# Performance work log

Hardware: AMD Instinct MI355X
Metric: run time of the kernel (lower is better)

## Reference

```python
import jax, jax.numpy as jnp
import numpy as np

IN_DIM = 512
OUT_DIM = 512


def setup_inputs() -> dict:
    key = jax.random.key(0)
    ks = jax.random.split(key, 7)
    B, S = 4, 2048
    scale = 1.0 / np.sqrt(IN_DIM)
    X = jax.random.normal(ks[0], (B, S, IN_DIM), dtype=jnp.float32)
    Wq = jax.random.normal(ks[1], (IN_DIM, OUT_DIM), dtype=jnp.float32) * scale
    Wk = jax.random.normal(ks[2], (IN_DIM, OUT_DIM), dtype=jnp.float32) * scale
    Wv = jax.random.normal(ks[3], (IN_DIM, OUT_DIM), dtype=jnp.float32) * scale
    bq = jnp.zeros((OUT_DIM,), dtype=jnp.float32)
    bk = jnp.zeros((OUT_DIM,), dtype=jnp.float32)
    bv = jnp.zeros((OUT_DIM,), dtype=jnp.float32)
    return {"X": X, "Wq": Wq, "bq": bq, "Wk": Wk, "bk": bk, "Wv": Wv, "bv": bv}


def reference(X, Wq, bq, Wk, bk, Wv, bv):
    # Q/K/V projections: [B,S,in] @ [in,out] -> [B,S,out]
    Q = X @ Wq + bq
    K = X @ Wk + bk
    V = X @ Wv + bv
    d_k = jnp.asarray(Q.shape[-1], Q.dtype)
    # scores: [B,S,S] = QK^T / sqrt(d_k)
    scores = jnp.einsum('bsd,btd->bst', Q, K) / jnp.sqrt(d_k)
    attn = jax.nn.softmax(scores, axis=-1)
    # out: [B,S,out]
    return jnp.einsum('bst,btd->bsd', attn, V)
```

## Files before the change

kernel.cpp:

```cpp
#include <hip/hip_runtime.h>
#include <hip/hip_bf16.h>
#include <stdint.h>

#define SEQ   2048
#define DIM   512
#define BATCH 4

typedef __attribute__((ext_vector_type(8))) short  short8;
typedef __attribute__((ext_vector_type(4))) float  floatx4;

static __device__ __forceinline__ unsigned short f2b(float f) {
  return __builtin_bit_cast(unsigned short, __float2bfloat16(f));
}

static __device__ __forceinline__ void gll16(const void* g, void* l) {
  __builtin_amdgcn_global_load_lds(
      (__attribute__((address_space(1))) void*)(uintptr_t)g,
      (__attribute__((address_space(3))) void*)l, 16, 0, 0);
}


template <int AF, int BF, int WM, int WN, int KC, int PH, int KIT>
__device__ __forceinline__ void fgemm_8p(
    const char* __restrict__ A, int rtA0, int TKA,
    const char* __restrict__ B, int rtB0, int TKB,
    char* lds, floatx4 (&acc)[AF / WM][BF / WN])
{
  constexpr int AWF  = AF / WM, BWF = BF / WN;
  constexpr int SLOT = (AF + BF) * KC * 1024;
  constexpr int L    = KC * (AF / 8 + BF / 8);
  constexpr int AC   = AWF / PH;
  static_assert(KIT >= 3, "pipeline needs >=3 K-slots");
  static_assert(AWF % PH == 0 && L % PH == 0, "phase split must divide");
  const int tid = threadIdx.x;
  const int w = tid >> 6, l = tid & 63;
  const int wm = w % WM, wn = w / WM;

  auto stage_part = [&](int slot, int kt, int p) {
    char* dst = lds + slot * SLOT;
#pragma unroll
    for (int g = p * (L / PH); g < (p + 1) * (L / PH); ++g) {
      if (g < KC * (AF / 8)) {
        const int c = g / (AF / 8), q = g % (AF / 8);
        const int f = q * 8 + w;
        gll16(A + (((size_t)(rtA0 + f) * TKA + kt * KC + c) << 10) + l * 16,
              dst + (c * AF + f) * 1024 + l * 16);
      } else {
        const int h = g - KC * (AF / 8);
        const int c = h / (BF / 8), q = h % (BF / 8);
        const int f = q * 8 + w;
        gll16(B + (((size_t)(rtB0 + f) * TKB + kt * KC + c) << 10) + l * 16,
              dst + (KC * AF + c * BF + f) * 1024 + l * 16);
      }
    }
  };
  auto stage_all = [&](int slot, int kt) {
#pragma unroll
    for (int p = 0; p < PH; ++p) stage_part(slot, kt, p);
  };

  stage_all(0, 0); stage_all(1, 1); stage_all(2, 2);
  asm volatile("s_waitcnt vmcnt(%0) lgkmcnt(0)\ns_barrier" :: "n"(2 * L) : "memory");

  short8 bf[KC][BWF];
#pragma unroll 4
  for (int kt = 0; kt < KIT; ++kt) {
    const char* bA = lds + (kt & 3) * SLOT;
    const char* bB = bA + KC * AF * 1024;
#pragma unroll
    for (int p = 0; p < PH; ++p) {
      short8 af[KC][AC];
#pragma unroll
      for (int c = 0; c < KC; ++c)
#pragma unroll
        for (int i = 0; i < AC; ++i)
          af[c][i] = *(const short8*)(bA + (c * AF + wm * AWF + p * AC + i) * 1024 + l * 16);
      if (p == 0) {
#pragma unroll
        for (int c = 0; c < KC; ++c)
#pragma unroll
          for (int j = 0; j < BWF; ++j)
            bf[c][j] = *(const short8*)(bB + (c * BF + wn * BWF + j) * 1024 + l * 16);
      }
      if (kt + 3 < KIT) stage_part((kt + 3) & 3, kt + 3, p);

      asm volatile("s_barrier" ::: "memory");
      asm volatile("s_waitcnt lgkmcnt(0)" ::: "memory");
      __builtin_amdgcn_s_setprio(1);
#pragma unroll
      for (int c = 0; c < KC; ++c)
#pragma unroll
        for (int i = 0; i < AC; ++i)
#pragma unroll
          for (int j = 0; j < BWF; ++j)
            acc[p * AC + i][j] = __builtin_amdgcn_mfma_f32_16x16x32_bf16(
                af[c][i], bf[c][j], acc[p * AC + i][j], 0, 0, 0);
      __builtin_amdgcn_s_setprio(0);

      if (p == PH - 1) {
        if (kt + 3 < KIT)
          asm volatile("s_waitcnt vmcnt(%0)\ns_barrier" :: "n"(2 * L) : "memory");
        else if (kt + 2 < KIT)
          asm volatile("s_waitcnt vmcnt(%0)\ns_barrier" :: "n"(L) : "memory");
        else if (kt + 1 < KIT)
          asm volatile("s_waitcnt vmcnt(0)\ns_barrier" ::: "memory");
      } else {
        asm volatile("s_barrier" ::: "memory");
      }
    }
  }
}

__global__ __launch_bounds__(256) void setup_kernel(
    const float* __restrict__ X, const float* __restrict__ Wq,
    const float* __restrict__ Wk, const float* __restrict__ Wv,
    short8* __restrict__ XbF, short8* __restrict__ WF,
    float* __restrict__ rowsum)
{
  const int flat = blockIdx.x * 256 + threadIdx.x;
  {
    const int tile = flat >> 6, l = flat & 63;
    const int row = (tile >> 4) * 16 + (l & 15);
    const int k0  = (tile & 15) * 32 + (l >> 4) * 8;
    const float4 v0 = *(const float4*)(X + (size_t)row * DIM + k0);
    const float4 v1 = *(const float4*)(X + (size_t)row * DIM + k0 + 4);
    short8 o;
    o[0] = (short)f2b(v0.x); o[1] = (short)f2b(v0.y);
    o[2] = (short)f2b(v0.z); o[3] = (short)f2b(v0.w);
    o[4] = (short)f2b(v1.x); o[5] = (short)f2b(v1.y);
    o[6] = (short)f2b(v1.z); o[7] = (short)f2b(v1.w);
    XbF[flat] = o;
  }
  if (flat < 3 * 32768) {
    const int z = flat >> 15, within = flat & 32767;
    const float* W = (z == 0) ? Wq : (z == 1) ? Wk : Wv;
    const int tile = within >> 6, l = within & 63;
    const int n  = (tile >> 4) * 16 + (l & 15);
    const int k0 = (tile & 15) * 32 + (l >> 4) * 8;
    short8 o;
#pragma unroll
    for (int e = 0; e < 8; ++e)
      o[e] = (short)f2b(W[(size_t)(k0 + e) * DIM + n]);
    WF[flat] = o;
  }
  if (flat < 2048) ((float4*)rowsum)[flat] = float4{0.f, 0.f, 0.f, 0.f};
}

__global__ __launch_bounds__(512, 2) void qkv_kernel(
    const short8* __restrict__ XbF, const short8* __restrict__ WF,
    const float* __restrict__ bq, const float* __restrict__ bk,
    const float* __restrict__ bv,
    unsigned short* __restrict__ QF, unsigned short* __restrict__ KF,
    unsigned short* __restrict__ VF)
{
  __shared__ char lds[131072];
  const int z = blockIdx.z, job = blockIdx.x;
  const int lane = threadIdx.x & 63, w = threadIdx.x >> 6;
  const int wm = w & 1, wn = w >> 1;
  const int x = job & 31, y = job >> 5;
  const char* Xc = (const char*)XbF;
  const char* Wc = (const char*)WF;
  floatx4 acc[8][4] = {};

  if (z < 2) {
    fgemm_8p<16, 16, 2, 4, 1, 2, 16>(Wc + (size_t)z * 524288, y * 16, 16,
                                     Xc, x * 16, 16, lds, acc);
    const float* bias = z ? bk : bq;
    unsigned short* OF = z ? KF : QF;
    const int dbase = y * 256 + wm * 128;
    const int sbase = x * 256 + wn * 64;
#pragma unroll
    for (int i = 0; i < 8; ++i) {
      const int d0 = dbase + i * 16 + (lane >> 4) * 4;
      const float4 b4 = *(const float4*)(bias + d0);
#pragma unroll
      for (int j = 0; j < 4; ++j) {
        const int s = sbase + j * 16 + (lane & 15);
        ushort4 pk;
        pk.x = f2b(acc[i][j][0] + b4.x);
        pk.y = f2b(acc[i][j][1] + b4.y);
        pk.z = f2b(acc[i][j][2] + b4.z);
        pk.w = f2b(acc[i][j][3] + b4.w);
        *(ushort4*)(OF + (size_t)((s >> 4) * 16 + (d0 >> 5)) * 512 +
                    ((((d0 & 31) >> 3) << 4) | (s & 15)) * 8 + (d0 & 7)) = pk;
      }
    }
  } else {
    fgemm_8p<16, 16, 2, 4, 1, 2, 16>(Xc, x * 16, 16,
                                     Wc + 2 * 524288, y * 16, 16, lds, acc);
    const int sbase = x * 256 + wm * 128;
    const int dbase = y * 256 + wn * 64;
#pragma unroll
    for (int i = 0; i < 8; ++i) {
      const int s0 = sbase + i * 16 + (lane >> 4) * 4;
      const int bt = s0 >> 11, t0 = s0 & 2047;
#pragma unroll
      for (int j = 0; j < 4; ++j) {
        const int d = dbase + j * 16 + (lane & 15);
        const float bn = bv[d];
        ushort4 pk;
        pk.x = f2b(acc[i][j][0] + bn);
        pk.y = f2b(acc[i][j][1] + bn);
        pk.z = f2b(acc[i][j][2] + bn);
        pk.w = f2b(acc[i][j][3] + bn);
        *(ushort4*)(VF + (size_t)bt * DIM * SEQ +
                    (size_t)((d >> 4) * 64 + (t0 >> 5)) * 512 +
                    ((((t0 & 31) >> 3) << 4) | (d & 15)) * 8 + (t0 & 7)) = pk;
      }
    }
  }
}

__global__ __launch_bounds__(512, 2) void scores_kernel(
    const unsigned short* __restrict__ QF, const unsigned short* __restrict__ KF,
    unsigned short* __restrict__ ScF, float* __restrict__ rowsum)
{
  __shared__ char lds[131072];
  const int b = blockIdx.z, x = blockIdx.x, y = blockIdx.y;
  const int lane = threadIdx.x & 63, w = threadIdx.x >> 6;
  const int wm = w & 1, wn = w >> 1;
  floatx4 acc[8][4] = {};
  fgemm_8p<16, 16, 2, 4, 1, 2, 16>((const char*)KF + (size_t)b * 2097152, y * 16, 16,
                                   (const char*)QF + (size_t)b * 2097152, x * 16, 16,
                                   lds, acc);

  unsigned short* S = ScF + (size_t)b * SEQ * SEQ;
  const float scale = 0.044194173824159216f;
  const int tbase = y * 256 + wm * 128;
  const int sbase = x * 256 + wn * 64;
  float colsum[4] = {0.f, 0.f, 0.f, 0.f};
#pragma unroll
  for (int i = 0; i < 8; ++i) {
    const int t0 = tbase + i * 16 + (lane >> 4) * 4;
#pragma unroll
    for (int j = 0; j < 4; ++j) {
      const int s = sbase + j * 16 + (lane & 15);
      float e0 = __expf(acc[i][j][0] * scale);
      float e1 = __expf(acc[i][j][1] * scale);
      float e2 = __expf(acc[i][j][2] * scale);
      float e3 = __expf(acc[i][j][3] * scale);
      colsum[j] += (e0 + e1) + (e2 + e3);
      ushort4 pk;
      pk.x = f2b(e0); pk.y = f2b(e1); pk.z = f2b(e2); pk.w = f2b(e3);
      *(ushort4*)(S + (size_t)((s >> 4) * 64 + (t0 >> 5)) * 512 +
                  ((((t0 & 31) >> 3) << 4) | (s & 15)) * 8 + (t0 & 7)) = pk;
    }
  }
#pragma unroll
  for (int j = 0; j < 4; ++j) {
    colsum[j] += __shfl_xor(colsum[j], 16, 64);
    colsum[j] += __shfl_xor(colsum[j], 32, 64);
  }
  if (lane < 16) {
#pragma unroll
    for (int j = 0; j < 4; ++j)
      atomicAdd(rowsum + b * SEQ + sbase + j * 16 + lane, colsum[j]);
  }
}

__global__ __launch_bounds__(512, 2) void pv_kernel(
    const unsigned short* __restrict__ ScF, const unsigned short* __restrict__ VF,
    const float* __restrict__ rowsum, float* __restrict__ out)
{
  __shared__ char lds[131072];
  const int b = blockIdx.z, x = blockIdx.x, y = blockIdx.y;
  const int lane = threadIdx.x & 63, w = threadIdx.x >> 6;
  const int wm = w & 1, wn = w >> 1;
  floatx4 acc[4][2] = {};
  fgemm_8p<8, 8, 2, 4, 2, 1, 32>((const char*)ScF + (size_t)b * 8388608, x * 8, 64,
                                 (const char*)VF + (size_t)b * 2097152, y * 8, 64,
                                 lds, acc);

  const int mbase = x * 128 + wm * 64;
  const int dbase = y * 128 + wn * 32;
#pragma unroll
  for (int i = 0; i < 4; ++i) {
    const int m0 = mbase + i * 16 + (lane >> 4) * 4;
    const float4 rs = *(const float4*)(rowsum + b * SEQ + m0);
    const float inv0 = 1.f / rs.x, inv1 = 1.f / rs.y, inv2 = 1.f / rs.z, inv3 = 1.f / rs.w;
#pragma unroll
    for (int j = 0; j < 2; ++j) {
      const int d = dbase + j * 16 + (lane & 15);
      float* o = out + ((size_t)b * SEQ + m0) * DIM + d;
      o[0 * DIM] = acc[i][j][0] * inv0;
      o[1 * DIM] = acc[i][j][1] * inv1;
      o[2 * DIM] = acc[i][j][2] * inv2;
      o[3 * DIM] = acc[i][j][3] * inv3;
    }
  }
}

extern "C" void kernel_launch(void* const* d_in, const int* in_sizes, int n_in,
                              void* d_out, int out_size, void* d_ws, size_t ws_size,
                              hipStream_t stream) {
  const float* X  = (const float*)d_in[0];
  const float* Wq = (const float*)d_in[1];
  const float* bq = (const float*)d_in[2];
  const float* Wk = (const float*)d_in[3];
  const float* bk = (const float*)d_in[4];
  const float* Wv = (const float*)d_in[5];
  const float* bv = (const float*)d_in[6];
  float* out = (float*)d_out;
  char* ws = (char*)d_ws;

  short8* XbF = (short8*)(ws + 0);
  short8* WF  = (short8*)(ws + 8388608);
  char*   QF  = ws + 9961472;
  char*   KF  = ws + 18350080;
  char*   VF  = ws + 26738688;
  char*   ScF = ws + 35127296;
  float*  rowsum = (float*)(ws + 68681728);

  setup_kernel<<<dim3(2048), 256, 0, stream>>>(X, Wq, Wk, Wv, XbF, WF, rowsum);
  qkv_kernel<<<dim3(64, 1, 3), 512, 0, stream>>>(
      XbF, WF, bq, bk, bv,
      (unsigned short*)QF, (unsigned short*)KF, (unsigned short*)VF);
  scores_kernel<<<dim3(8, 8, 4), 512, 0, stream>>>(
      (const unsigned short*)QF, (const unsigned short*)KF,
      (unsigned short*)ScF, rowsum);
  pv_kernel<<<dim3(16, 4, 4), 512, 0, stream>>>(
      (const unsigned short*)ScF, (const unsigned short*)VF, rowsum, out);
}
```

Baseline: 140.7 us.

## Fuse attention stages into one cooperative persistent kernel with grid syncs

The four kernels (conversion, QKV projection, scores plus exp, PV) become a single cooperative kernel of 256 blocks that separates the stages with grid-wide syncs, removing launch gaps between kernels. Row sums no longer use atomicAdd into a zeroed buffer: each block writes partial sums into a buffer that reuses the space of the bf16 X copy, and the PV stage reduces the 16 partials into reciprocals in LDS. The old multi-kernel path is kept as a fallback if the cooperative launch fails. In exchange, idle blocks during the QKV stage and the cost of grid syncs must be absorbed, and every block must fit co-resident.

```diff
diff --git a/kernel.cpp b/kernel.cpp
--- a/kernel.cpp
+++ b/kernel.cpp
@@ -1,6 +1,9 @@
 #include <hip/hip_runtime.h>
 #include <hip/hip_bf16.h>
+#include <hip/hip_cooperative_groups.h>
 #include <stdint.h>
+
+namespace cg = cooperative_groups;
 
 #define SEQ   2048
 #define DIM   512
@@ -111,11 +114,216 @@
   }
 }
 
+
+static __device__ __forceinline__ void do_setup(
+    int blk, const float* __restrict__ X, const float* __restrict__ Wq,
+    const float* __restrict__ Wk, const float* __restrict__ Wv,
+    short8* __restrict__ XbF, short8* __restrict__ WF)
+{
+#pragma unroll
+  for (int u = 0; u < 4; ++u) {
+    const int flat = blk * 2048 + u * 512 + (int)threadIdx.x;
+    const int tile = flat >> 6, l = flat & 63;
+    const int row = (tile >> 4) * 16 + (l & 15);
+    const int k0  = (tile & 15) * 32 + (l >> 4) * 8;
+    const float4 v0 = *(const float4*)(X + (size_t)row * DIM + k0);
+    const float4 v1 = *(const float4*)(X + (size_t)row * DIM + k0 + 4);
+    short8 o;
+    o[0] = (short)f2b(v0.x); o[1] = (short)f2b(v0.y);
+    o[2] = (short)f2b(v0.z); o[3] = (short)f2b(v0.w);
+    o[4] = (short)f2b(v1.x); o[5] = (short)f2b(v1.y);
+    o[6] = (short)f2b(v1.z); o[7] = (short)f2b(v1.w);
+    XbF[flat] = o;
+  }
+  const int fl = blk * 512 + (int)threadIdx.x;
+  if (fl < 3 * 32768) {
+    const int z = fl >> 15, within = fl & 32767;
+    const float* W = (z == 0) ? Wq : (z == 1) ? Wk : Wv;
+    const int tile = within >> 6, l = within & 63;
+    const int n  = (tile >> 4) * 16 + (l & 15);
+    const int k0 = (tile & 15) * 32 + (l >> 4) * 8;
+    short8 o;
+#pragma unroll
+    for (int e = 0; e < 8; ++e)
+      o[e] = (short)f2b(W[(size_t)(k0 + e) * DIM + n]);
+    WF[fl] = o;
+  }
+}
+
+static __device__ __forceinline__ void do_qkv(
+    int z, int job, char* lds, const short8* __restrict__ XbF,
+    const short8* __restrict__ WF, const float* __restrict__ bq,
+    const float* __restrict__ bk, const float* __restrict__ bv,
+    unsigned short* __restrict__ QF, unsigned short* __restrict__ KF,
+    unsigned short* __restrict__ VF)
+{
+  const int lane = threadIdx.x & 63, w = threadIdx.x >> 6;
+  const int wm = w & 1, wn = w >> 1;
+  const int x = job & 31, y = job >> 5;
+  const char* Xc = (const char*)XbF;
+  const char* Wc = (const char*)WF;
+  floatx4 acc[8][4] = {};
+
+  if (z < 2) {
+    fgemm_8p<16, 16, 2, 4, 1, 2, 16>(Wc + (size_t)z * 524288, y * 16, 16,
+                                     Xc, x * 16, 16, lds, acc);
+    const float* bias = z ? bk : bq;
+    unsigned short* OF = z ? KF : QF;
+    const int dbase = y * 256 + wm * 128;
+    const int sbase = x * 256 + wn * 64;
+#pragma unroll
+    for (int i = 0; i < 8; ++i) {
+      const int d0 = dbase + i * 16 + (lane >> 4) * 4;
+      const float4 b4 = *(const float4*)(bias + d0);
+#pragma unroll
+      for (int j = 0; j < 4; ++j) {
+        const int s = sbase + j * 16 + (lane & 15);
+        ushort4 pk;
+        pk.x = f2b(acc[i][j][0] + b4.x);
+        pk.y = f2b(acc[i][j][1] + b4.y);
+        pk.z = f2b(acc[i][j][2] + b4.z);
+        pk.w = f2b(acc[i][j][3] + b4.w);
+        *(ushort4*)(OF + (size_t)((s >> 4) * 16 + (d0 >> 5)) * 512 +
+                    ((((d0 & 31) >> 3) << 4) | (s & 15)) * 8 + (d0 & 7)) = pk;
+      }
+    }
+  } else {
+    fgemm_8p<16, 16, 2, 4, 1, 2, 16>(Xc, x * 16, 16,
+                                     Wc + 2 * 524288, y * 16, 16, lds, acc);
+    const int sbase = x * 256 + wm * 128;
+    const int dbase = y * 256 + wn * 64;
+#pragma unroll
+    for (int i = 0; i < 8; ++i) {
+      const int s0 = sbase + i * 16 + (lane >> 4) * 4;
+      const int bt = s0 >> 11, t0 = s0 & 2047;
+#pragma unroll
+      for (int j = 0; j < 4; ++j) {
+        const int d = dbase + j * 16 + (lane & 15);
+        const float bn = bv[d];
+        ushort4 pk;
+        pk.x = f2b(acc[i][j][0] + bn);
+        pk.y = f2b(acc[i][j][1] + bn);
+        pk.z = f2b(acc[i][j][2] + bn);
+        pk.w = f2b(acc[i][j][3] + bn);
+        *(ushort4*)(VF + (size_t)bt * DIM * SEQ +
+                    (size_t)((d >> 4) * 64 + (t0 >> 5)) * 512 +
+                    ((((t0 & 31) >> 3) << 4) | (d & 15)) * 8 + (t0 & 7)) = pk;
+      }
+    }
+  }
+}
+
+static __device__ __forceinline__ void do_scores(
+    int b, int x, int y, char* lds, const unsigned short* __restrict__ QF,
+    const unsigned short* __restrict__ KF, unsigned short* __restrict__ ScF,
+    float* __restrict__ prow)
+{
+  const int lane = threadIdx.x & 63, w = threadIdx.x >> 6;
+  const int wm = w & 1, wn = w >> 1;
+  floatx4 acc[8][4] = {};
+  fgemm_8p<16, 16, 2, 4, 1, 2, 16>((const char*)KF + (size_t)b * 2097152, y * 16, 16,
+                                   (const char*)QF + (size_t)b * 2097152, x * 16, 16,
+                                   lds, acc);
+
+  unsigned short* S = ScF + (size_t)b * SEQ * SEQ;
+  const float scale = 0.044194173824159216f;
+  const int tbase = y * 256 + wm * 128;
+  const int sbase = x * 256 + wn * 64;
+  float colsum[4] = {0.f, 0.f, 0.f, 0.f};
+#pragma unroll
+  for (int i = 0; i < 8; ++i) {
+    const int t0 = tbase + i * 16 + (lane >> 4) * 4;
+#pragma unroll
+    for (int j = 0; j < 4; ++j) {
+      const int s = sbase + j * 16 + (lane & 15);
+      float e0 = __expf(acc[i][j][0] * scale);
+      float e1 = __expf(acc[i][j][1] * scale);
+      float e2 = __expf(acc[i][j][2] * scale);
+      float e3 = __expf(acc[i][j][3] * scale);
+      colsum[j] += (e0 + e1) + (e2 + e3);
+      ushort4 pk;
+      pk.x = f2b(e0); pk.y = f2b(e1); pk.z = f2b(e2); pk.w = f2b(e3);
+      *(ushort4*)(S + (size_t)((s >> 4) * 64 + (t0 >> 5)) * 512 +
+                  ((((t0 & 31) >> 3) << 4) | (s & 15)) * 8 + (t0 & 7)) = pk;
+    }
+  }
+#pragma unroll
+  for (int j = 0; j < 4; ++j) {
+    colsum[j] += __shfl_xor(colsum[j], 16, 64);
+    colsum[j] += __shfl_xor(colsum[j], 32, 64);
+  }
+  if (lane < 16) {
+    float* dst = prow + ((size_t)(y * 2 + wm) * BATCH + b) * SEQ + sbase + lane;
+#pragma unroll
+    for (int j = 0; j < 4; ++j) dst[j * 16] = colsum[j];
+  }
+}
+
+static __device__ __forceinline__ void do_pv(
+    int b, int x, int y, char* lds, float* rinv,
+    const unsigned short* __restrict__ ScF, const unsigned short* __restrict__ VF,
+    const float* __restrict__ prow, float* __restrict__ out)
+{
+  const int t = threadIdx.x;
+  if (t < 128) {
+    const int s = x * 128 + t;
+    float r = 0.f;
+#pragma unroll
+    for (int q = 0; q < 16; ++q) r += prow[((size_t)q * BATCH + b) * SEQ + s];
+    rinv[t] = 1.f / r;
+  }
+  const int lane = threadIdx.x & 63, w = threadIdx.x >> 6;
+  const int wm = w & 1, wn = w >> 1;
+  floatx4 acc[4][2] = {};
+  fgemm_8p<8, 8, 2, 4, 2, 1, 32>((const char*)ScF + (size_t)b * 8388608, x * 8, 64,
+                                 (const char*)VF + (size_t)b * 2097152, y * 8, 64,
+                                 lds, acc);
+
+  const int mbase = x * 128 + wm * 64;
+  const int dbase = y * 128 + wn * 32;
+#pragma unroll
+  for (int i = 0; i < 4; ++i) {
+    const int r0 = wm * 64 + i * 16 + (lane >> 4) * 4;
+    const int m0 = mbase + i * 16 + (lane >> 4) * 4;
+    const float inv0 = rinv[r0], inv1 = rinv[r0 + 1], inv2 = rinv[r0 + 2], inv3 = rinv[r0 + 3];
+#pragma unroll
+    for (int j = 0; j < 2; ++j) {
+      const int d = dbase + j * 16 + (lane & 15);
+      float* o = out + ((size_t)b * SEQ + m0) * DIM + d;
+      o[0 * DIM] = acc[i][j][0] * inv0;
+      o[1 * DIM] = acc[i][j][1] * inv1;
+      o[2 * DIM] = acc[i][j][2] * inv2;
+      o[3 * DIM] = acc[i][j][3] * inv3;
+    }
+  }
+}
+
+__global__ __launch_bounds__(512, 2) void mega_kernel(
+    const float* X, const float* Wq, const float* Wk, const float* Wv,
+    const float* bq, const float* bk, const float* bv,
+    short8* XbF, short8* WF, unsigned short* QF, unsigned short* KF,
+    unsigned short* VF, unsigned short* ScF, float* prow, float* out)
+{
+  __shared__ char lds[131072];
+  __shared__ float rinv[128];
+  cg::grid_group grid = cg::this_grid();
+  const int blk = blockIdx.x;
+
+  do_setup(blk, X, Wq, Wk, Wv, XbF, WF);
+  grid.sync();
+  if (blk < 192) do_qkv(blk >> 6, blk & 63, lds, XbF, WF, bq, bk, bv, QF, KF, VF);
+  grid.sync();
+  { const int b = blk >> 6, r = blk & 63;
+    do_scores(b, r & 7, r >> 3, lds, QF, KF, ScF, prow); }
+  grid.sync();
+  { const int b = blk >> 6, r = blk & 63;
+    do_pv(b, r >> 2, r & 3, lds, rinv, ScF, VF, prow, out); }
+}
+
 __global__ __launch_bounds__(256) void setup_kernel(
     const float* __restrict__ X, const float* __restrict__ Wq,
     const float* __restrict__ Wk, const float* __restrict__ Wv,
-    short8* __restrict__ XbF, short8* __restrict__ WF,
-    float* __restrict__ rowsum)
+    short8* __restrict__ XbF, short8* __restrict__ WF)
 {
   const int flat = blockIdx.x * 256 + threadIdx.x;
   {
@@ -143,7 +351,6 @@
       o[e] = (short)f2b(W[(size_t)(k0 + e) * DIM + n]);
     WF[flat] = o;
   }
-  if (flat < 2048) ((float4*)rowsum)[flat] = float4{0.f, 0.f, 0.f, 0.f};
 }
 
 __global__ __launch_bounds__(512, 2) void qkv_kernel(
@@ -154,140 +361,24 @@
     unsigned short* __restrict__ VF)
 {
   __shared__ char lds[131072];
-  const int z = blockIdx.z, job = blockIdx.x;
-  const int lane = threadIdx.x & 63, w = threadIdx.x >> 6;
-  const int wm = w & 1, wn = w >> 1;
-  const int x = job & 31, y = job >> 5;
-  const char* Xc = (const char*)XbF;
-  const char* Wc = (const char*)WF;
-  floatx4 acc[8][4] = {};
-
-  if (z < 2) {
-    fgemm_8p<16, 16, 2, 4, 1, 2, 16>(Wc + (size_t)z * 524288, y * 16, 16,
-                                     Xc, x * 16, 16, lds, acc);
-    const float* bias = z ? bk : bq;
-    unsigned short* OF = z ? KF : QF;
-    const int dbase = y * 256 + wm * 128;
-    const int sbase = x * 256 + wn * 64;
-#pragma unroll
-    for (int i = 0; i < 8; ++i) {
-      const int d0 = dbase + i * 16 + (lane >> 4) * 4;
-      const float4 b4 = *(const float4*)(bias + d0);
-#pragma unroll
-      for (int j = 0; j < 4; ++j) {
-        const int s = sbase + j * 16 + (lane & 15);
-        ushort4 pk;
-        pk.x = f2b(acc[i][j][0] + b4.x);
-        pk.y = f2b(acc[i][j][1] + b4.y);
-        pk.z = f2b(acc[i][j][2] + b4.z);
-        pk.w = f2b(acc[i][j][3] + b4.w);
-        *(ushort4*)(OF + (size_t)((s >> 4) * 16 + (d0 >> 5)) * 512 +
-                    ((((d0 & 31) >> 3) << 4) | (s & 15)) * 8 + (d0 & 7)) = pk;
-      }
-    }
-  } else {
-    fgemm_8p<16, 16, 2, 4, 1, 2, 16>(Xc, x * 16, 16,
-                                     Wc + 2 * 524288, y * 16, 16, lds, acc);
-    const int sbase = x * 256 + wm * 128;
-    const int dbase = y * 256 + wn * 64;
-#pragma unroll
-    for (int i = 0; i < 8; ++i) {
-      const int s0 = sbase + i * 16 + (lane >> 4) * 4;
-      const int bt = s0 >> 11, t0 = s0 & 2047;
-#pragma unroll
-      for (int j = 0; j < 4; ++j) {
-        const int d = dbase + j * 16 + (lane & 15);
-        const float bn = bv[d];
-        ushort4 pk;
-        pk.x = f2b(acc[i][j][0] + bn);
-        pk.y = f2b(acc[i][j][1] + bn);
-        pk.z = f2b(acc[i][j][2] + bn);
-        pk.w = f2b(acc[i][j][3] + bn);
-        *(ushort4*)(VF + (size_t)bt * DIM * SEQ +
-                    (size_t)((d >> 4) * 64 + (t0 >> 5)) * 512 +
-                    ((((t0 & 31) >> 3) << 4) | (d & 15)) * 8 + (t0 & 7)) = pk;
-      }
-    }
-  }
+  do_qkv(blockIdx.z, blockIdx.x, lds, XbF, WF, bq, bk, bv, QF, KF, VF);
 }
 
 __global__ __launch_bounds__(512, 2) void scores_kernel(
     const unsigned short* __restrict__ QF, const unsigned short* __restrict__ KF,
-    unsigned short* __restrict__ ScF, float* __restrict__ rowsum)
+    unsigned short* __restrict__ ScF, float* __restrict__ prow)
 {
   __shared__ char lds[131072];
-  const int b = blockIdx.z, x = blockIdx.x, y = blockIdx.y;
-  const int lane = threadIdx.x & 63, w = threadIdx.x >> 6;
-  const int wm = w & 1, wn = w >> 1;
-  floatx4 acc[8][4] = {};
-  fgemm_8p<16, 16, 2, 4, 1, 2, 16>((const char*)KF + (size_t)b * 2097152, y * 16, 16,
-                                   (const char*)QF + (size_t)b * 2097152, x * 16, 16,
-                                   lds, acc);
-
-  unsigned short* S = ScF + (size_t)b * SEQ * SEQ;
-  const float scale = 0.044194173824159216f;
-  const int tbase = y * 256 + wm * 128;
-  const int sbase = x * 256 + wn * 64;
-  float colsum[4] = {0.f, 0.f, 0.f, 0.f};
-#pragma unroll
-  for (int i = 0; i < 8; ++i) {
-    const int t0 = tbase + i * 16 + (lane >> 4) * 4;
-#pragma unroll
-    for (int j = 0; j < 4; ++j) {
-      const int s = sbase + j * 16 + (lane & 15);
-      float e0 = __expf(acc[i][j][0] * scale);
-      float e1 = __expf(acc[i][j][1] * scale);
-      float e2 = __expf(acc[i][j][2] * scale);
-      float e3 = __expf(acc[i][j][3] * scale);
-      colsum[j] += (e0 + e1) + (e2 + e3);
-      ushort4 pk;
-      pk.x = f2b(e0); pk.y = f2b(e1); pk.z = f2b(e2); pk.w = f2b(e3);
-      *(ushort4*)(S + (size_t)((s >> 4) * 64 + (t0 >> 5)) * 512 +
-                  ((((t0 & 31) >> 3) << 4) | (s & 15)) * 8 + (t0 & 7)) = pk;
-    }
-  }
-#pragma unroll
-  for (int j = 0; j < 4; ++j) {
-    colsum[j] += __shfl_xor(colsum[j], 16, 64);
-    colsum[j] += __shfl_xor(colsum[j], 32, 64);
-  }
-  if (lane < 16) {
-#pragma unroll
-    for (int j = 0; j < 4; ++j)
-      atomicAdd(rowsum + b * SEQ + sbase + j * 16 + lane, colsum[j]);
-  }
+  do_scores(blockIdx.z, blockIdx.x, blockIdx.y, lds, QF, KF, ScF, prow);
 }
 
 __global__ __launch_bounds__(512, 2) void pv_kernel(
     const unsigned short* __restrict__ ScF, const unsigned short* __restrict__ VF,
-    const float* __restrict__ rowsum, float* __restrict__ out)
+    const float* __restrict__ prow, float* __restrict__ out)
 {
   __shared__ char lds[131072];
-  const int b = blockIdx.z, x = blockIdx.x, y = blockIdx.y;
-  const int lane = threadIdx.x & 63, w = threadIdx.x >> 6;
-  const int wm = w & 1, wn = w >> 1;
-  floatx4 acc[4][2] = {};
-  fgemm_8p<8, 8, 2, 4, 2, 1, 32>((const char*)ScF + (size_t)b * 8388608, x * 8, 64,
-                                 (const char*)VF + (size_t)b * 2097152, y * 8, 64,
-                                 lds, acc);
-
-  const int mbase = x * 128 + wm * 64;
-  const int dbase = y * 128 + wn * 32;
-#pragma unroll
-  for (int i = 0; i < 4; ++i) {
-    const int m0 = mbase + i * 16 + (lane >> 4) * 4;
-    const float4 rs = *(const float4*)(rowsum + b * SEQ + m0);
-    const float inv0 = 1.f / rs.x, inv1 = 1.f / rs.y, inv2 = 1.f / rs.z, inv3 = 1.f / rs.w;
-#pragma unroll
-    for (int j = 0; j < 2; ++j) {
-      const int d = dbase + j * 16 + (lane & 15);
-      float* o = out + ((size_t)b * SEQ + m0) * DIM + d;
-      o[0 * DIM] = acc[i][j][0] * inv0;
-      o[1 * DIM] = acc[i][j][1] * inv1;
-      o[2 * DIM] = acc[i][j][2] * inv2;
-      o[3 * DIM] = acc[i][j][3] * inv3;
-    }
-  }
+  __shared__ float rinv[128];
+  do_pv(blockIdx.z, blockIdx.x, blockIdx.y, lds, rinv, ScF, VF, prow, out);
 }
 
 extern "C" void kernel_launch(void* const* d_in, const int* in_sizes, int n_in,
@@ -304,20 +395,26 @@
   char* ws = (char*)d_ws;
 
   short8* XbF = (short8*)(ws + 0);
+  float*  prow = (float*)(ws + 0);
   short8* WF  = (short8*)(ws + 8388608);
-  char*   QF  = ws + 9961472;
-  char*   KF  = ws + 18350080;
-  char*   VF  = ws + 26738688;
-  char*   ScF = ws + 35127296;
-  float*  rowsum = (float*)(ws + 68681728);
-
-  setup_kernel<<<dim3(2048), 256, 0, stream>>>(X, Wq, Wk, Wv, XbF, WF, rowsum);
-  qkv_kernel<<<dim3(64, 1, 3), 512, 0, stream>>>(
-      XbF, WF, bq, bk, bv,
-      (unsigned short*)QF, (unsigned short*)KF, (unsigned short*)VF);
-  scores_kernel<<<dim3(8, 8, 4), 512, 0, stream>>>(
-      (const unsigned short*)QF, (const unsigned short*)KF,
-      (unsigned short*)ScF, rowsum);
-  pv_kernel<<<dim3(16, 4, 4), 512, 0, stream>>>(
-      (const unsigned short*)ScF, (const unsigned short*)VF, rowsum, out);
-}
+  unsigned short* QF  = (unsigned short*)(ws + 9961472);
+  unsigned short* KF  = (unsigned short*)(ws + 18350080);
+  unsigned short* VF  = (unsigned short*)(ws + 26738688);
+  unsigned short* ScF = (unsigned short*)(ws + 35127296);
+
+  void* args[] = {
+    (void*)&X, (void*)&Wq, (void*)&Wk, (void*)&Wv,
+    (void*)&bq, (void*)&bk, (void*)&bv,
+    (void*)&XbF, (void*)&WF, (void*)&QF, (void*)&KF,
+    (void*)&VF, (void*)&ScF, (void*)&prow, (void*)&out
+  };
+  hipError_t e = hipLaunchCooperativeKernel(
+      (const void*)mega_kernel, dim3(256), dim3(512), args, 0, stream);
+  if (e != hipSuccess) {
+    (void)hipGetLastError();
+    setup_kernel<<<dim3(2048), 256, 0, stream>>>(X, Wq, Wk, Wv, XbF, WF);
+    qkv_kernel<<<dim3(64, 1, 3), 512, 0, stream>>>(XbF, WF, bq, bk, bv, QF, KF, VF);
+    scores_kernel<<<dim3(8, 8, 4), 512, 0, stream>>>(QF, KF, ScF, prow);
+    pv_kernel<<<dim3(16, 4, 4), 512, 0, stream>>>(ScF, VF, prow, out);
+  }
+}
```

Measured after the change: 260.8 us. 1.85x slower.

## Remap grids for XCD-local L2 reuse and replace rowsum atomics with partial sums

Applied to the files above, without the earlier changes.

Flattens the grids of the qkv, scores and pv kernels into 1D and remaps block indices so that blocks sharing operands (same batch, same rows) land on the same XCD, which is meant to improve L2 reuse. The scores kernel now writes per-tile partial row sums into a buffer instead of using atomicAdd, and pv reduces those 16 partials per row into LDS before the GEMM. This drops the zeroing step in setup and the atomic traffic. In exchange, the partial-sum buffer reuses the XbF workspace region, which is safe only because XbF is dead after qkv, and pv does some extra global reads.

```diff
diff --git a/kernel.cpp b/kernel.cpp
--- a/kernel.cpp
+++ b/kernel.cpp
@@ -114,8 +114,7 @@
 __global__ __launch_bounds__(256) void setup_kernel(
     const float* __restrict__ X, const float* __restrict__ Wq,
     const float* __restrict__ Wk, const float* __restrict__ Wv,
-    short8* __restrict__ XbF, short8* __restrict__ WF,
-    float* __restrict__ rowsum)
+    short8* __restrict__ XbF, short8* __restrict__ WF)
 {
   const int flat = blockIdx.x * 256 + threadIdx.x;
   {
@@ -143,7 +142,6 @@
       o[e] = (short)f2b(W[(size_t)(k0 + e) * DIM + n]);
     WF[flat] = o;
   }
-  if (flat < 2048) ((float4*)rowsum)[flat] = float4{0.f, 0.f, 0.f, 0.f};
 }
 
 __global__ __launch_bounds__(512, 2) void qkv_kernel(
@@ -154,10 +152,13 @@
     unsigned short* __restrict__ VF)
 {
   __shared__ char lds[131072];
-  const int z = blockIdx.z, job = blockIdx.x;
+  const int n = blockIdx.x;
+  const int xcd = n & 7, i = n >> 3;
+  const int x = xcd + 8 * (i & 3);
+  const int zy = i >> 2;
+  const int z = zy >> 1, y = zy & 1;
   const int lane = threadIdx.x & 63, w = threadIdx.x >> 6;
   const int wm = w & 1, wn = w >> 1;
-  const int x = job & 31, y = job >> 5;
   const char* Xc = (const char*)XbF;
   const char* Wc = (const char*)WF;
   floatx4 acc[8][4] = {};
@@ -170,17 +171,17 @@
     const int dbase = y * 256 + wm * 128;
     const int sbase = x * 256 + wn * 64;
 #pragma unroll
-    for (int i = 0; i < 8; ++i) {
-      const int d0 = dbase + i * 16 + (lane >> 4) * 4;
+    for (int i2 = 0; i2 < 8; ++i2) {
+      const int d0 = dbase + i2 * 16 + (lane >> 4) * 4;
       const float4 b4 = *(const float4*)(bias + d0);
 #pragma unroll
       for (int j = 0; j < 4; ++j) {
         const int s = sbase + j * 16 + (lane & 15);
         ushort4 pk;
-        pk.x = f2b(acc[i][j][0] + b4.x);
-        pk.y = f2b(acc[i][j][1] + b4.y);
-        pk.z = f2b(acc[i][j][2] + b4.z);
-        pk.w = f2b(acc[i][j][3] + b4.w);
+        pk.x = f2b(acc[i2][j][0] + b4.x);
+        pk.y = f2b(acc[i2][j][1] + b4.y);
+        pk.z = f2b(acc[i2][j][2] + b4.z);
+        pk.w = f2b(acc[i2][j][3] + b4.w);
         *(ushort4*)(OF + (size_t)((s >> 4) * 16 + (d0 >> 5)) * 512 +
                     ((((d0 & 31) >> 3) << 4) | (s & 15)) * 8 + (d0 & 7)) = pk;
       }
@@ -191,18 +192,18 @@
     const int sbase = x * 256 + wm * 128;
     const int dbase = y * 256 + wn * 64;
 #pragma unroll
-    for (int i = 0; i < 8; ++i) {
-      const int s0 = sbase + i * 16 + (lane >> 4) * 4;
+    for (int i2 = 0; i2 < 8; ++i2) {
+      const int s0 = sbase + i2 * 16 + (lane >> 4) * 4;
       const int bt = s0 >> 11, t0 = s0 & 2047;
 #pragma unroll
       for (int j = 0; j < 4; ++j) {
         const int d = dbase + j * 16 + (lane & 15);
         const float bn = bv[d];
         ushort4 pk;
-        pk.x = f2b(acc[i][j][0] + bn);
-        pk.y = f2b(acc[i][j][1] + bn);
-        pk.z = f2b(acc[i][j][2] + bn);
-        pk.w = f2b(acc[i][j][3] + bn);
+        pk.x = f2b(acc[i2][j][0] + bn);
+        pk.y = f2b(acc[i2][j][1] + bn);
+        pk.z = f2b(acc[i2][j][2] + bn);
+        pk.w = f2b(acc[i2][j][3] + bn);
         *(ushort4*)(VF + (size_t)bt * DIM * SEQ +
                     (size_t)((d >> 4) * 64 + (t0 >> 5)) * 512 +
                     ((((t0 & 31) >> 3) << 4) | (d & 15)) * 8 + (t0 & 7)) = pk;
@@ -213,10 +214,14 @@
 
 __global__ __launch_bounds__(512, 2) void scores_kernel(
     const unsigned short* __restrict__ QF, const unsigned short* __restrict__ KF,
-    unsigned short* __restrict__ ScF, float* __restrict__ rowsum)
+    unsigned short* __restrict__ ScF, float* __restrict__ prow)
 {
   __shared__ char lds[131072];
-  const int b = blockIdx.z, x = blockIdx.x, y = blockIdx.y;
+  const int n = blockIdx.x;
+  const int xcd = n & 7, i = n >> 3;
+  const int b = xcd >> 1;
+  const int x = (xcd & 1) * 4 + (i & 3);
+  const int y = i >> 2;
   const int lane = threadIdx.x & 63, w = threadIdx.x >> 6;
   const int wm = w & 1, wn = w >> 1;
   floatx4 acc[8][4] = {};
@@ -230,15 +235,15 @@
   const int sbase = x * 256 + wn * 64;
   float colsum[4] = {0.f, 0.f, 0.f, 0.f};
 #pragma unroll
-  for (int i = 0; i < 8; ++i) {
-    const int t0 = tbase + i * 16 + (lane >> 4) * 4;
+  for (int i2 = 0; i2 < 8; ++i2) {
+    const int t0 = tbase + i2 * 16 + (lane >> 4) * 4;
 #pragma unroll
     for (int j = 0; j < 4; ++j) {
       const int s = sbase + j * 16 + (lane & 15);
-      float e0 = __expf(acc[i][j][0] * scale);
-      float e1 = __expf(acc[i][j][1] * scale);
-      float e2 = __expf(acc[i][j][2] * scale);
-      float e3 = __expf(acc[i][j][3] * scale);
+      float e0 = __expf(acc[i2][j][0] * scale);
+      float e1 = __expf(acc[i2][j][1] * scale);
+      float e2 = __expf(acc[i2][j][2] * scale);
+      float e3 = __expf(acc[i2][j][3] * scale);
       colsum[j] += (e0 + e1) + (e2 + e3);
       ushort4 pk;
       pk.x = f2b(e0); pk.y = f2b(e1); pk.z = f2b(e2); pk.w = f2b(e3);
@@ -252,18 +257,31 @@
     colsum[j] += __shfl_xor(colsum[j], 32, 64);
   }
   if (lane < 16) {
-#pragma unroll
-    for (int j = 0; j < 4; ++j)
-      atomicAdd(rowsum + b * SEQ + sbase + j * 16 + lane, colsum[j]);
+    float* dst = prow + ((size_t)(y * 2 + wm) * BATCH + b) * SEQ + sbase + lane;
+#pragma unroll
+    for (int j = 0; j < 4; ++j) dst[j * 16] = colsum[j];
   }
 }
 
 __global__ __launch_bounds__(512, 2) void pv_kernel(
     const unsigned short* __restrict__ ScF, const unsigned short* __restrict__ VF,
-    const float* __restrict__ rowsum, float* __restrict__ out)
+    const float* __restrict__ prow, float* __restrict__ out)
 {
   __shared__ char lds[131072];
-  const int b = blockIdx.z, x = blockIdx.x, y = blockIdx.y;
+  __shared__ float rinv[128];
+  const int n = blockIdx.x;
+  const int xcd = n & 7, i = n >> 3;
+  const int b = xcd >> 1;
+  const int x = (xcd & 1) * 8 + (i & 7);
+  const int y = i >> 3;
+  const int t = threadIdx.x;
+  if (t < 128) {
+    const int s = x * 128 + t;
+    float r = 0.f;
+#pragma unroll
+    for (int q = 0; q < 16; ++q) r += prow[((size_t)q * BATCH + b) * SEQ + s];
+    rinv[t] = 1.f / r;
+  }
   const int lane = threadIdx.x & 63, w = threadIdx.x >> 6;
   const int wm = w & 1, wn = w >> 1;
   floatx4 acc[4][2] = {};
@@ -274,18 +292,18 @@
   const int mbase = x * 128 + wm * 64;
   const int dbase = y * 128 + wn * 32;
 #pragma unroll
-  for (int i = 0; i < 4; ++i) {
-    const int m0 = mbase + i * 16 + (lane >> 4) * 4;
-    const float4 rs = *(const float4*)(rowsum + b * SEQ + m0);
-    const float inv0 = 1.f / rs.x, inv1 = 1.f / rs.y, inv2 = 1.f / rs.z, inv3 = 1.f / rs.w;
+  for (int i2 = 0; i2 < 4; ++i2) {
+    const int r0 = wm * 64 + i2 * 16 + (lane >> 4) * 4;
+    const int m0 = mbase + i2 * 16 + (lane >> 4) * 4;
+    const float inv0 = rinv[r0], inv1 = rinv[r0 + 1], inv2 = rinv[r0 + 2], inv3 = rinv[r0 + 3];
 #pragma unroll
     for (int j = 0; j < 2; ++j) {
       const int d = dbase + j * 16 + (lane & 15);
       float* o = out + ((size_t)b * SEQ + m0) * DIM + d;
-      o[0 * DIM] = acc[i][j][0] * inv0;
-      o[1 * DIM] = acc[i][j][1] * inv1;
-      o[2 * DIM] = acc[i][j][2] * inv2;
-      o[3 * DIM] = acc[i][j][3] * inv3;
+      o[0 * DIM] = acc[i2][j][0] * inv0;
+      o[1 * DIM] = acc[i2][j][1] * inv1;
+      o[2 * DIM] = acc[i2][j][2] * inv2;
+      o[3 * DIM] = acc[i2][j][3] * inv3;
     }
   }
 }
@@ -304,20 +322,15 @@
   char* ws = (char*)d_ws;
 
   short8* XbF = (short8*)(ws + 0);
+  float*  prow = (float*)(ws + 0);
   short8* WF  = (short8*)(ws + 8388608);
-  char*   QF  = ws + 9961472;
-  char*   KF  = ws + 18350080;
-  char*   VF  = ws + 26738688;
-  char*   ScF = ws + 35127296;
-  float*  rowsum = (float*)(ws + 68681728);
-
-  setup_kernel<<<dim3(2048), 256, 0, stream>>>(X, Wq, Wk, Wv, XbF, WF, rowsum);
-  qkv_kernel<<<dim3(64, 1, 3), 512, 0, stream>>>(
-      XbF, WF, bq, bk, bv,
-      (unsigned short*)QF, (unsigned short*)KF, (unsigned short*)VF);
-  scores_kernel<<<dim3(8, 8, 4), 512, 0, stream>>>(
-      (const unsigned short*)QF, (const unsigned short*)KF,
-      (unsigned short*)ScF, rowsum);
-  pv_kernel<<<dim3(16, 4, 4), 512, 0, stream>>>(
-      (const unsigned short*)ScF, (const unsigned short*)VF, rowsum, out);
-}
+  unsigned short* QF  = (unsigned short*)(ws + 9961472);
+  unsigned short* KF  = (unsigned short*)(ws + 18350080);
+  unsigned short* VF  = (unsigned short*)(ws + 26738688);
+  unsigned short* ScF = (unsigned short*)(ws + 35127296);
+
+  setup_kernel<<<dim3(2048), 256, 0, stream>>>(X, Wq, Wk, Wv, XbF, WF);
+  qkv_kernel<<<dim3(192), 512, 0, stream>>>(XbF, WF, bq, bk, bv, QF, KF, VF);
+  scores_kernel<<<dim3(256), 512, 0, stream>>>(QF, KF, ScF, prow);
+  pv_kernel<<<dim3(256), 512, 0, stream>>>(ScF, VF, prow, out);
+}
```

New measurement: 142.8 us. Within noise of the previous version (+1.5%).
